# Kernel optimization log

Measured on AMD Instinct MI355X. Metric: run time of the kernel, lower is better.

The kernel has to match this reference:

```python
import jax, jax.numpy as jnp
import numpy as np

B, N, C = 2, 2048, 768
H = 12
HD = C // H
SCALE = HD ** -0.5


def setup_inputs() -> dict:
    key = jax.random.key(0)
    ks = jax.random.split(key, 5)
    s = 1.0 / np.sqrt(C)
    return {
        "x": jax.random.normal(ks[0], (B, N, C), dtype=jnp.float32),
        "Wq": jax.random.normal(ks[1], (C, C), dtype=jnp.float32) * s,
        "Wk": jax.random.normal(ks[2], (C, C), dtype=jnp.float32) * s,
        "Wv": jax.random.normal(ks[3], (C, C), dtype=jnp.float32) * s,
        "Wo": jax.random.normal(ks[4], (C, C), dtype=jnp.float32) * s,
        "bo": jnp.zeros((C,), dtype=jnp.float32),
    }


def reference(x, Wq, Wk, Wv, Wo, bo):
    b, n, c = x.shape
    # projections (equinox Linear: y = W @ x, i.e. x @ W.T); split heads -> [b, h, n, hd]
    q = (x @ Wq.T).reshape(b, n, H, HD).transpose(0, 2, 1, 3)
    k = (x @ Wk.T).reshape(b, n, H, HD).transpose(0, 2, 1, 3)
    v = (x @ Wv.T).reshape(b, n, H, HD).transpose(0, 2, 1, 3)
    # full O(N^2) score matrix, scaled dot-product
    scores = jnp.einsum("bhqd,bhkd->bhqk", q, k) * SCALE  # [b, h, n, n]
    probs = jax.nn.softmax(scores, axis=-1)
    # attn_drop = 0.0 -> identity
    out = jnp.einsum("bhqk,bhkd->bhqd", probs, v)  # [b, h, n, hd]
    out = out.transpose(0, 2, 1, 3).reshape(b, n, c)
    # output projection (proj_drop = 0.0 -> identity)
    return out @ Wo.T + bo
```

## Files before the change

kernel.cpp:

```cpp
#include <hip/hip_runtime.h>
#include <hip/hip_bf16.h>
#include <cstdint>

typedef __bf16 bf16;
typedef bf16 bf16x8 __attribute__((ext_vector_type(8)));
typedef float f32x4 __attribute__((ext_vector_type(4)));
typedef uint32_t u32;

#define MFMA16(a, b, c) __builtin_amdgcn_mfma_f32_16x16x32_bf16(a, b, c, 0, 0, 0)

static constexpr int Bb = 2, Hh = 12, Nn = 2048, Cc = 768, HD = 64;
static constexpr float SCALE_L2E = 0.125f * 1.4426950408889634f;

__device__ inline u32 pkbf(float a, float b) {
    union { struct { uint16_t lo, hi; } s; u32 w; } u;
    u.s.lo = __builtin_bit_cast(uint16_t, (bf16)a);
    u.s.hi = __builtin_bit_cast(uint16_t, (bf16)b);
    return u.w;
}

__device__ __forceinline__ size_t fidx(int bh, int n, int hd) {
    return ((size_t)(bh * 128 + (n >> 4)) * 2 + (hd >> 5)) * 512 +
           (size_t)(((hd >> 3) & 3) * 128 + (n & 15) * 8 + (hd & 7));
}
__device__ __forceinline__ size_t vidx(int bh, int n, int hd) {
    return (((size_t)(bh * 32 + (n >> 6)) * 4 + (hd >> 4)) * 2 + ((n >> 5) & 1)) * 512 +
           (size_t)(((n >> 3) & 3) * 128 + (hd & 15) * 8 + (n & 7));
}

__device__ __forceinline__ void stage16(const bf16* g, bf16* l) {
    __builtin_amdgcn_global_load_lds(
        (const __attribute__((address_space(1))) void*)g,
        (__attribute__((address_space(3))) void*)l, 16, 0, 0);
}

#define VMWAIT(N) do { asm volatile("s_waitcnt vmcnt(" #N ")" ::); \
                       __builtin_amdgcn_sched_barrier(0); } while (0)

__global__ __launch_bounds__(256) void cvt_all(const float* __restrict__ x,
                                               const float* __restrict__ wq,
                                               const float* __restrict__ wk,
                                               const float* __restrict__ wv,
                                               const float* __restrict__ wo,
                                               bf16* __restrict__ xb,
                                               bf16* __restrict__ wqkv,
                                               bf16* __restrict__ wob) {
    const int b = blockIdx.x;
    const float* src;
    bf16* dst;
    int i;
    if (b < 1536) {
        src = x; dst = xb; i = b * 256 + threadIdx.x;
    } else {
        const int wbid  = b - 1536;
        const int which = wbid / 288;
        src = which == 0 ? wq : which == 1 ? wk : which == 2 ? wv : wo;
        dst = which == 3 ? wob : wqkv + (size_t)which * 589824;
        i = (wbid % 288) * 256 + threadIdx.x;
    }
    const float4* p = reinterpret_cast<const float4*>(src) + (size_t)i * 2;
    float4 v0 = p[0], v1 = p[1];
    bf16x8 o;
    o[0] = (bf16)v0.x; o[1] = (bf16)v0.y; o[2] = (bf16)v0.z; o[3] = (bf16)v0.w;
    o[4] = (bf16)v1.x; o[5] = (bf16)v1.y; o[6] = (bf16)v1.z; o[7] = (bf16)v1.w;
    reinterpret_cast<bf16x8*>(dst)[i] = o;
}

__global__ __launch_bounds__(256, 3) void gemm_qkv(const bf16* __restrict__ X,
                                                   const bf16* __restrict__ W,
                                                   bf16* __restrict__ QF,
                                                   bf16* __restrict__ KF,
                                                   bf16* __restrict__ VF) {
    const int m0      = blockIdx.x * 128;
    const int j00     = blockIdx.y * 128;
    const int grp     = blockIdx.y / 6;
    const int colbase = (blockIdx.y % 6) * 128;
    const int w   = threadIdx.x >> 6;
    const int wr  = w >> 1;
    const int wc  = w & 1;
    const int l   = threadIdx.x & 63;
    const int lr  = l & 15;
    const int lg  = l >> 4;

    __shared__ bf16 lsA[2][128 * 32];
    __shared__ bf16 lsB[2][128 * 32];

    const int lrow = l >> 2;
    const int lcol = (l & 3) * 8;

    auto STAGE = [&](int buf, int kk) {
#pragma unroll
        for (int i = 0; i < 2; i++) {
            const int s = w * 2 + i;
            stage16(X + (size_t)(m0 + s * 16 + lrow) * Cc + kk + lcol, &lsA[buf][s * 512]);
            stage16(W + (size_t)(j00 + s * 16 + lrow) * Cc + kk + lcol, &lsB[buf][s * 512]);
        }
    };

    f32x4 acc[4][4] = {};

    STAGE(0, 0);
    __syncthreads();
    int cur = 0;
#pragma unroll 1
    for (int it = 0; it < 24; ++it) {
        if (it < 23) STAGE(cur ^ 1, (it + 1) * 32);
        bf16x8 a[4], b[4];
#pragma unroll
        for (int r = 0; r < 4; r++)
            a[r] = *reinterpret_cast<const bf16x8*>(&lsA[cur][(wr * 64 + r * 16 + lr) * 32 + lg * 8]);
#pragma unroll
        for (int c = 0; c < 4; c++)
            b[c] = *reinterpret_cast<const bf16x8*>(&lsB[cur][(wc * 64 + c * 16 + lr) * 32 + lg * 8]);
        __builtin_amdgcn_s_setprio(1);
#pragma unroll
        for (int r = 0; r < 4; r++)
#pragma unroll
            for (int c = 0; c < 4; c++)
                acc[r][c] = MFMA16(a[r], b[c], acc[r][c]);
        __builtin_amdgcn_s_setprio(0);
        __syncthreads();
        cur ^= 1;
    }

#pragma unroll
    for (int r = 0; r < 4; r++)
#pragma unroll
        for (int c = 0; c < 4; c++)
#pragma unroll
            for (int j = 0; j < 4; j++) {
                const int m   = m0 + wr * 64 + r * 16 + lg * 4 + j;
                const int col = colbase + wc * 64 + c * 16 + lr;
                const int bb = m >> 11, n = m & 2047;
                const int h = col >> 6, hd = col & 63;
                const int bh = bb * Hh + h;
                const float v = acc[r][c][j];
                if (grp == 0) {
                    QF[fidx(bh, n, hd)] = (bf16)(v * SCALE_L2E);
                } else if (grp == 1) {
                    KF[fidx(bh, n, hd)] = (bf16)v;
                } else {
                    VF[vidx(bh, n, hd)] = (bf16)v;
                }
            }
}

__global__ __launch_bounds__(256) void gemm_proj(const bf16* __restrict__ X,
                                                 const bf16* __restrict__ W,
                                                 const float* __restrict__ bias,
                                                 float* __restrict__ Y) {
    const int m0 = blockIdx.x * 64;
    const int j0 = blockIdx.y * 64;
    const int w  = threadIdx.x >> 6;
    const int l  = threadIdx.x & 63;
    const int lr = l & 15;
    const int lg = l >> 4;

    __shared__ bf16 lsA[2][64 * 32];
    __shared__ bf16 lsB[2][64 * 32];

    const int lrow = l >> 2;
    const int lcol = (l & 3) * 8;

    auto STAGE = [&](int buf, int kk) {
        stage16(X + (size_t)(m0 + w * 16 + lrow) * Cc + kk + lcol, &lsA[buf][w * 512]);
        stage16(W + (size_t)(j0 + w * 16 + lrow) * Cc + kk + lcol, &lsB[buf][w * 512]);
    };

    f32x4 acc[4] = {};

    STAGE(0, 0);
    __syncthreads();
    int cur = 0;
#pragma unroll 1
    for (int it = 0; it < 24; ++it) {
        if (it < 23) STAGE(cur ^ 1, (it + 1) * 32);
        bf16x8 a = *reinterpret_cast<const bf16x8*>(&lsA[cur][(w * 16 + lr) * 32 + lg * 8]);
        bf16x8 b[4];
#pragma unroll
        for (int c = 0; c < 4; c++)
            b[c] = *reinterpret_cast<const bf16x8*>(&lsB[cur][(c * 16 + lr) * 32 + lg * 8]);
        __builtin_amdgcn_s_setprio(1);
#pragma unroll
        for (int c = 0; c < 4; c++)
            acc[c] = MFMA16(a, b[c], acc[c]);
        __builtin_amdgcn_s_setprio(0);
        __syncthreads();
        cur ^= 1;
    }

    const int mw = m0 + w * 16;
#pragma unroll
    for (int c = 0; c < 4; c++)
#pragma unroll
        for (int j = 0; j < 4; j++) {
            const int m   = mw + lg * 4 + j;
            const int col = j0 + c * 16 + lr;
            Y[(size_t)m * Cc + col] = acc[c][j] + bias[col];
        }
}

__global__ __launch_bounds__(256, 3) void attn_kernel(const bf16* __restrict__ QF,
                                                      const bf16* __restrict__ KF,
                                                      const bf16* __restrict__ VF,
                                                      bf16* __restrict__ AO) {
    const int bid = (blockIdx.x & 7) * 96 + (blockIdx.x >> 3);
    const int qb  = bid & 31;
    const int bh  = bid >> 5;
    const int tid = threadIdx.x;
    const int wid = tid >> 6;
    const int l   = tid & 63;
    const int lr  = l & 15;
    const int lg  = l >> 4;

    __shared__ bf16 smem[20992];
    bf16* kbuf  = smem;
    bf16* vbuf  = smem + 8192;
    u32*  p_lds = reinterpret_cast<u32*>(smem + 16384);

    f32x4 acc[4] = {};
    f32x4 accs = {0.f, 0.f, 0.f, 0.f};

    const bf16* Qp = QF + ((size_t)(bh * 128 + qb * 4 + wid) * 2) * 512 + l * 8;
    const bf16x8 qf0 = *reinterpret_cast<const bf16x8*>(Qp);
    const bf16x8 qf1 = *reinterpret_cast<const bf16x8*>(Qp + 512);

    bf16x8 ONES;
#pragma unroll
    for (int i = 0; i < 8; i++) ONES[i] = (bf16)1.0f;

    auto STAGE_K = [&](int buf, int t) {
        const size_t tb = ((size_t)bh * 256 + t * 8) * 512;
#pragma unroll
        for (int i = 0; i < 2; i++) {
            const int s = wid * 2 + i;
            stage16(KF + tb + (size_t)s * 512 + l * 8, &kbuf[buf * 4096 + s * 512]);
        }
    };
    auto STAGE_V = [&](int buf, int t) {
        const size_t tb = ((size_t)bh * 256 + t * 8) * 512;
#pragma unroll
        for (int i = 0; i < 2; i++) {
            const int s = wid * 2 + i;
            stage16(VF + tb + (size_t)s * 512 + l * 8, &vbuf[buf * 4096 + s * 512]);
        }
    };

    const f32x4 fz = {0.f, 0.f, 0.f, 0.f};

    STAGE_K(0, 0);
    STAGE_V(0, 0);

#pragma unroll 1
    for (int t = 0; t < 32; ++t) {
        const int cur = t & 1;
        VMWAIT(0);
        __builtin_amdgcn_s_barrier();

        bf16x8 kf[8];
#pragma unroll
        for (int s8 = 0; s8 < 8; s8++)
            kf[s8] = *reinterpret_cast<const bf16x8*>(&kbuf[cur * 4096 + s8 * 512 + l * 8]);
        if (t < 31) STAGE_K(cur ^ 1, t + 1);

        f32x4 s[4];
        __builtin_amdgcn_s_setprio(1);
#pragma unroll
        for (int st = 0; st < 4; st++) {
            s[st] = MFMA16(kf[st * 2], qf0, fz);
            s[st] = MFMA16(kf[st * 2 + 1], qf1, s[st]);
        }
        __builtin_amdgcn_s_setprio(0);

        float p[4][4];
#pragma unroll
        for (int st = 0; st < 4; st++)
#pragma unroll
            for (int j = 0; j < 4; j++)
                p[st][j] = exp2f(s[st][j]);
#pragma unroll
        for (int st = 0; st < 4; st++) {
            u32 w0 = pkbf(p[st][0], p[st][1]);
            u32 w1 = pkbf(p[st][2], p[st][3]);
            *reinterpret_cast<uint2*>(&p_lds[wid * 576 + lr * 36 + st * 8 + lg * 2]) = make_uint2(w0, w1);
        }
        asm volatile("s_waitcnt lgkmcnt(0)" ::: "memory");
        __builtin_amdgcn_sched_barrier(0);
        const bf16x8 pa0 = *reinterpret_cast<const bf16x8*>(&p_lds[wid * 576 + lr * 36 + lg * 4]);
        const bf16x8 pa1 = *reinterpret_cast<const bf16x8*>(&p_lds[wid * 576 + lr * 36 + 16 + lg * 4]);

        bf16x8 vf[8];
#pragma unroll
        for (int s8 = 0; s8 < 8; s8++)
            vf[s8] = *reinterpret_cast<const bf16x8*>(&vbuf[cur * 4096 + s8 * 512 + l * 8]);
        if (t < 31) STAGE_V(cur ^ 1, t + 1);

        __builtin_amdgcn_s_setprio(1);
#pragma unroll
        for (int c = 0; c < 4; c++) {
            acc[c] = MFMA16(vf[c * 2], pa0, acc[c]);
            acc[c] = MFMA16(vf[c * 2 + 1], pa1, acc[c]);
        }
        accs = MFMA16(ONES, pa0, accs);
        accs = MFMA16(ONES, pa1, accs);
        __builtin_amdgcn_s_setprio(0);
    }
    __builtin_amdgcn_s_barrier();

    float* o_lds = reinterpret_cast<float*>(smem) + wid * 1088;
    const float rinv = 1.0f / accs[0];
#pragma unroll
    for (int c = 0; c < 4; c++)
#pragma unroll
        for (int j = 0; j < 4; j++)
            o_lds[(c * 16 + lg * 4 + j) * 17 + lr] = acc[c][j] * rinv;
    asm volatile("s_waitcnt lgkmcnt(0)" ::: "memory");
    __builtin_amdgcn_sched_barrier(0);

    const int bb = bh / Hh, h = bh % Hh;
    const int q0 = qb * 64 + wid * 16;
    const int qq = l >> 2, dc = (l & 3) * 16;
    bf16x8 o0, o1;
#pragma unroll
    for (int dd = 0; dd < 8; dd++) o0[dd] = (bf16)o_lds[(dc + dd) * 17 + qq];
#pragma unroll
    for (int dd = 0; dd < 8; dd++) o1[dd] = (bf16)o_lds[(dc + 8 + dd) * 17 + qq];
    bf16* dst = AO + ((size_t)(bb * Nn) + q0 + qq) * Cc + h * 64 + dc;
    *reinterpret_cast<bf16x8*>(dst) = o0;
    *reinterpret_cast<bf16x8*>(dst + 8) = o1;
}

extern "C" void kernel_launch(void* const* d_in, const int* in_sizes, int n_in,
                              void* d_out, int out_size, void* d_ws, size_t ws_size,
                              hipStream_t stream) {
    const float* x  = (const float*)d_in[0];
    const float* Wq = (const float*)d_in[1];
    const float* Wk = (const float*)d_in[2];
    const float* Wv = (const float*)d_in[3];
    const float* Wo = (const float*)d_in[4];
    const float* bo = (const float*)d_in[5];

    const size_t XB    = 0;
    const size_t WQKVB = XB + 6291456;
    const size_t WOB   = WQKVB + 3538944;
    const size_t QB    = WOB + 1179648;
    const size_t KB    = QB + 6291456;
    const size_t VTB   = KB + 6291456;
    const size_t AOB   = VTB + 6291456;
    const size_t NEED  = AOB + 6291456;
    if (ws_size < NEED) return;

    char* ws = (char*)d_ws;
    bf16* xb   = (bf16*)(ws + XB);
    bf16* wqkv = (bf16*)(ws + WQKVB);
    bf16* wob  = (bf16*)(ws + WOB);
    bf16* QF   = (bf16*)(ws + QB);
    bf16* KF   = (bf16*)(ws + KB);
    bf16* VF   = (bf16*)(ws + VTB);
    bf16* AOb  = (bf16*)(ws + AOB);

    cvt_all<<<2688, 256, 0, stream>>>(x, Wq, Wk, Wv, Wo, xb, wqkv, wob);

    gemm_qkv<<<dim3(32, 18), 256, 0, stream>>>(xb, wqkv, QF, KF, VF);

    attn_kernel<<<768, 256, 0, stream>>>(QF, KF, VF, AOb);

    gemm_proj<<<dim3(64, 12), 256, 0, stream>>>(AOb, wob, bo, (float*)d_out);
}
```

Baseline: 100.4 us.

## Load K tiles directly into registers and triple-buffer V in LDS

The attention inner loop no longer stages K through LDS. Each wave loads its K fragments straight into registers with global_load_dwordx4, prefetching the next tile right after the QK MFMAs. V moves to a three-slot LDS ring that is prefetched two tiles ahead, and the wait becomes vmcnt(2) so the newest V stage stays in flight across the barrier. This removes the LDS write/read round trip for K and deepens the V prefetch, at the cost of extra VGPRs for the register-resident K prefetch, which may pressure occupancy at three blocks per CU.

```diff
diff --git a/kernel.cpp b/kernel.cpp
--- a/kernel.cpp
+++ b/kernel.cpp
@@ -32,6 +32,10 @@
     __builtin_amdgcn_global_load_lds(
         (const __attribute__((address_space(1))) void*)g,
         (__attribute__((address_space(3))) void*)l, 16, 0, 0);
+}
+
+__device__ __forceinline__ void gload(bf16x8& d, const bf16* p) {
+    asm volatile("global_load_dwordx4 %0, %1, off" : "=v"(d) : "v"(p));
 }
 
 #define VMWAIT(N) do { asm volatile("s_waitcnt vmcnt(" #N ")" ::); \
@@ -213,10 +217,8 @@
     const int lr  = l & 15;
     const int lg  = l >> 4;
 
-    __shared__ bf16 smem[20992];
-    bf16* kbuf  = smem;
-    bf16* vbuf  = smem + 8192;
-    u32*  p_lds = reinterpret_cast<u32*>(smem + 16384);
+    __shared__ bf16 vbuf[3][4096];
+    __shared__ u32  p_lds[4][576];
 
     f32x4 acc[4] = {};
     f32x4 accs = {0.f, 0.f, 0.f, 0.f};
@@ -229,85 +231,81 @@
 #pragma unroll
     for (int i = 0; i < 8; i++) ONES[i] = (bf16)1.0f;
 
-    auto STAGE_K = [&](int buf, int t) {
+    bf16x8 ka[8];
+
+    auto loadK = [&](int t) {
+        const bf16* p = KF + ((size_t)bh * 256 + t * 8) * 512 + l * 8;
+#pragma unroll
+        for (int s = 0; s < 8; s++)
+            gload(ka[s], p + (size_t)s * 512);
+    };
+    auto stageV = [&](int slot, int t) {
         const size_t tb = ((size_t)bh * 256 + t * 8) * 512;
 #pragma unroll
         for (int i = 0; i < 2; i++) {
             const int s = wid * 2 + i;
-            stage16(KF + tb + (size_t)s * 512 + l * 8, &kbuf[buf * 4096 + s * 512]);
-        }
-    };
-    auto STAGE_V = [&](int buf, int t) {
-        const size_t tb = ((size_t)bh * 256 + t * 8) * 512;
-#pragma unroll
-        for (int i = 0; i < 2; i++) {
-            const int s = wid * 2 + i;
-            stage16(VF + tb + (size_t)s * 512 + l * 8, &vbuf[buf * 4096 + s * 512]);
+            stage16(VF + tb + (size_t)s * 512 + l * 8, &vbuf[slot][s * 512]);
         }
     };
 
     const f32x4 fz = {0.f, 0.f, 0.f, 0.f};
 
-    STAGE_K(0, 0);
-    STAGE_V(0, 0);
-
-#pragma unroll 1
-    for (int t = 0; t < 32; ++t) {
-        const int cur = t & 1;
-        VMWAIT(0);
-        __builtin_amdgcn_s_barrier();
-
-        bf16x8 kf[8];
-#pragma unroll
-        for (int s8 = 0; s8 < 8; s8++)
-            kf[s8] = *reinterpret_cast<const bf16x8*>(&kbuf[cur * 4096 + s8 * 512 + l * 8]);
-        if (t < 31) STAGE_K(cur ^ 1, t + 1);
-
+    auto BODY = [&](int t, bool prefetchK) {
         f32x4 s[4];
         __builtin_amdgcn_s_setprio(1);
 #pragma unroll
         for (int st = 0; st < 4; st++) {
-            s[st] = MFMA16(kf[st * 2], qf0, fz);
-            s[st] = MFMA16(kf[st * 2 + 1], qf1, s[st]);
+            s[st] = MFMA16(ka[st * 2], qf0, fz);
+            s[st] = MFMA16(ka[st * 2 + 1], qf1, s[st]);
         }
         __builtin_amdgcn_s_setprio(0);
-
-        float p[4][4];
-#pragma unroll
-        for (int st = 0; st < 4; st++)
-#pragma unroll
-            for (int j = 0; j < 4; j++)
-                p[st][j] = exp2f(s[st][j]);
+        if (prefetchK) loadK(t + 1);
+
 #pragma unroll
         for (int st = 0; st < 4; st++) {
-            u32 w0 = pkbf(p[st][0], p[st][1]);
-            u32 w1 = pkbf(p[st][2], p[st][3]);
-            *reinterpret_cast<uint2*>(&p_lds[wid * 576 + lr * 36 + st * 8 + lg * 2]) = make_uint2(w0, w1);
+            float p0 = exp2f(s[st][0]);
+            float p1 = exp2f(s[st][1]);
+            float p2 = exp2f(s[st][2]);
+            float p3 = exp2f(s[st][3]);
+            *reinterpret_cast<uint2*>(&p_lds[wid][lr * 36 + st * 8 + lg * 2]) =
+                make_uint2(pkbf(p0, p1), pkbf(p2, p3));
         }
         asm volatile("s_waitcnt lgkmcnt(0)" ::: "memory");
         __builtin_amdgcn_sched_barrier(0);
-        const bf16x8 pa0 = *reinterpret_cast<const bf16x8*>(&p_lds[wid * 576 + lr * 36 + lg * 4]);
-        const bf16x8 pa1 = *reinterpret_cast<const bf16x8*>(&p_lds[wid * 576 + lr * 36 + 16 + lg * 4]);
-
-        bf16x8 vf[8];
-#pragma unroll
-        for (int s8 = 0; s8 < 8; s8++)
-            vf[s8] = *reinterpret_cast<const bf16x8*>(&vbuf[cur * 4096 + s8 * 512 + l * 8]);
-        if (t < 31) STAGE_V(cur ^ 1, t + 1);
-
+        const bf16x8 pa0 = *reinterpret_cast<const bf16x8*>(&p_lds[wid][lr * 36 + lg * 4]);
+        const bf16x8 pa1 = *reinterpret_cast<const bf16x8*>(&p_lds[wid][lr * 36 + 16 + lg * 4]);
+
+        const bf16* vb = &vbuf[t % 3][l * 8];
         __builtin_amdgcn_s_setprio(1);
 #pragma unroll
         for (int c = 0; c < 4; c++) {
-            acc[c] = MFMA16(vf[c * 2], pa0, acc[c]);
-            acc[c] = MFMA16(vf[c * 2 + 1], pa1, acc[c]);
+            bf16x8 v0 = *reinterpret_cast<const bf16x8*>(vb + (c * 2) * 512);
+            bf16x8 v1 = *reinterpret_cast<const bf16x8*>(vb + (c * 2 + 1) * 512);
+            acc[c] = MFMA16(v0, pa0, acc[c]);
+            acc[c] = MFMA16(v1, pa1, acc[c]);
         }
         accs = MFMA16(ONES, pa0, accs);
         accs = MFMA16(ONES, pa1, accs);
         __builtin_amdgcn_s_setprio(0);
+    };
+
+    stageV(0, 0);
+    loadK(0);
+    stageV(1, 1);
+
+#pragma unroll 1
+    for (int t = 0; t < 31; ++t) {
+        VMWAIT(2);
+        __builtin_amdgcn_s_barrier();
+        BODY(t, true);
+        if (t <= 29) stageV((t + 2) % 3, t + 2);
     }
+    VMWAIT(0);
     __builtin_amdgcn_s_barrier();
-
-    float* o_lds = reinterpret_cast<float*>(smem) + wid * 1088;
+    BODY(31, false);
+    __builtin_amdgcn_s_barrier();
+
+    float* o_lds = reinterpret_cast<float*>(&vbuf[0][0]) + wid * 1088;
     const float rinv = 1.0f / accs[0];
 #pragma unroll
     for (int c = 0; c < 4; c++)
```

Measured after the change: 99.74 us. About the same (-0.7%).
